# Kernel tuning notes

Measured on AMD Instinct MI355X. Metric: run time of the kernel, lower is better.

The kernel has to match this reference:

```python
import jax, jax.numpy as jnp
import numpy as np

T, B, DG, DH, S = 48, 96, 192, 384, 3
LAM, ETA = 0.9, 0.5
LN_EPS = 1e-5

def layernorm(x, g, b):
    m = jnp.mean(x, axis=-1, keepdims=True)
    v = jnp.var(x, axis=-1, keepdims=True)
    return (x - m) * jax.lax.rsqrt(v + LN_EPS) * g + b

def setup_inputs() -> dict:
    key = jax.random.key(0)
    k0, k1, k2, k3 = jax.random.split(key, 4)
    z_seq = jax.random.normal(k0, (T, B, DG), jnp.float32)
    # kaiming-uniform-ish / xavier-ish scaling for realism
    W_h = jax.random.normal(k1, (DH, DH), jnp.float32) * (2.0 / DH) ** 0.5
    W_g = jax.random.normal(k2, (DH, DG), jnp.float32) * (1.0 / DG) ** 0.5
    b_h = jnp.zeros((DH,), jnp.float32)
    ln_g = jnp.ones((DH,), jnp.float32)
    ln_b = jnp.zeros((DH,), jnp.float32)
    alpha_fw = jax.random.uniform(k3, (1,), jnp.float32)  # cfg.alpha_fw (learned scalar)
    return dict(z_seq=z_seq, W_h=W_h, W_g=W_g, b_h=b_h, ln_g=ln_g, ln_b=ln_b, alpha_fw=alpha_fw)

def reference(z_seq, W_h, W_g, b_h, ln_g, ln_b, alpha_fw):
    # compute_k(): curvature of cosine gate
    k = jnp.where(alpha_fw >= 0,
                  1.0 + jax.nn.softplus(alpha_fw),
                  1.0 / (1.0 + jax.nn.softplus(-alpha_fw)))  # shape (1,)

    def step(carry, z_t):
        h, A = carry                                   # h: [B,DH], A: [B,DH,DH]
        h_base = h @ W_h.T + z_t @ W_g.T + b_h          # [B,DH]
        h_s = jax.nn.relu(layernorm(h_base, ln_g, ln_b))
        # inner fast-weight settling loop with cosine-similarity gate
        for _ in range(S):
            Ah = jnp.einsum('bij,bj->bi', A, h_s)       # bmm(A, h)
            dot = jnp.sum(h_s * Ah, axis=-1, keepdims=True)
            n1 = jnp.maximum(jnp.linalg.norm(h_s, axis=-1, keepdims=True), 1e-6)
            n2 = jnp.maximum(jnp.linalg.norm(Ah, axis=-1, keepdims=True), 1e-6)
            R = jnp.clip(dot / (n1 * n2), 0.0, 1.0)
            a = 1.0 - (1.0 - R) ** k                    # alpha_dyn, [B,1]
            h_s = jax.nn.relu(layernorm((1.0 - a * a) * h_base + a * Ah, ln_g, ln_b))
        h = h_s
        # Hebbian fast-weight update: A <- lambda*A + eta * h h^T
        A = LAM * A + ETA * jnp.einsum('bi,bj->bij', h, h)
        return (h, A), None

    Bn, Dh = z_seq.shape[1], W_h.shape[0]
    h0 = jnp.zeros((Bn, Dh), z_seq.dtype)
    A0 = jnp.zeros((Bn, Dh, Dh), z_seq.dtype)
    (h, A), _ = jax.lax.scan(step, (h0, A0), z_seq[:-1])

    # final (query) step: no gating, no A update, h_s = relu(LN(h_base + A h_s))
    z_t = z_seq[-1]
    h_base = h @ W_h.T + z_t @ W_g.T + b_h
    h = jax.nn.relu(layernorm(h_base, ln_g, ln_b))
    for _ in range(S):
        Ah = jnp.einsum('bij,bj->bi', A, h)
        h = jax.nn.relu(layernorm(h_base + Ah, ln_g, ln_b))
    return h
```

## Files before the change

kernel.cpp:

```cpp
#include <hip/hip_runtime.h>
#include <math.h>

#define TT    48
#define BB    96
#define DG    192
#define DH    384
#define NSTEP 47
#define SETI  3
#define NT    768
#define NWAVE 12
#define NOW   6
#define NG    48

typedef unsigned short ushort_t;
typedef float f32x2 __attribute__((ext_vector_type(2)));

template <int CTRL, int RM>
__device__ __forceinline__ float dppadd(float acc, float x) {
  int t = __builtin_amdgcn_update_dpp(0, __float_as_int(x), CTRL, RM, 0xF, false);
  return acc + __int_as_float(t);
}

__device__ __forceinline__ float row16_sum(float v) {
  v = dppadd<0x128, 0xF>(v, v);
  v = dppadd<0x124, 0xF>(v, v);
  v = dppadd<0x122, 0xF>(v, v);
  v = dppadd<0x121, 0xF>(v, v);
  return v;
}

__device__ __forceinline__ float wave_sum63(float v) {
  v = row16_sum(v);
  v = dppadd<0x142, 0xA>(v, v);
  v = dppadd<0x143, 0xC>(v, v);
  return v;
}

__device__ __forceinline__ float blo(unsigned u) {
  return __uint_as_float(u << 16);
}
__device__ __forceinline__ float bhi(unsigned u) {
  return __uint_as_float(u & 0xFFFF0000u);
}
__device__ __forceinline__ f32x2 pkfma(f32x2 a, f32x2 b, f32x2 c) {
  return __builtin_elementwise_fma(a, b, c);
}

template <bool FULL>
__device__ __forceinline__ void matvec(
    const float* __restrict__ Wh_f, const float* __restrict__ Wg_f,
    const ushort_t* __restrict__ Wh_b,
    const float* __restrict__ hprev, const float* __restrict__ zsh,
    const float* __restrict__ gzrow,
    const float (&bias)[8], float* __restrict__ hbs,
    float& s1, float& s2, int g, int lane16, bool with_h)
{
  f32x2 h2[12];
  if (with_h) {
    const float4* h4 = (const float4*)hprev;
#pragma unroll
    for (int c = 0; c < 6; ++c) {
      float4 hh = h4[lane16 + 16 * c];
      h2[2 * c]     = f32x2{hh.x, hh.y};
      h2[2 * c + 1] = f32x2{hh.z, hh.w};
    }
  }
  float4 zz[3];
  if (!FULL) {
    const float4* z4 = (const float4*)zsh;
#pragma unroll
    for (int c = 0; c < 3; ++c) zz[c] = z4[lane16 + 16 * c];
  }
#pragma unroll 2
  for (int p = 0; p < 8; ++p) {
    const int r = p * NG + g;
    f32x2 acc0 = {0.f, 0.f}, acc1 = {0.f, 0.f};
    float gzv = 0.f;
    if (FULL) {
      if (lane16 == 0) gzv = gzrow[r];
    } else {
      const float4* wg = (const float4*)Wg_f + (size_t)r * (DG / 4);
#pragma unroll
      for (int c = 0; c < 3; ++c) {
        float4 w = wg[lane16 + 16 * c];
        acc0 = pkfma(f32x2{w.x, w.y}, f32x2{zz[c].x, zz[c].y}, acc0);
        acc1 = pkfma(f32x2{w.z, w.w}, f32x2{zz[c].z, zz[c].w}, acc1);
      }
    }
    if (with_h) {
      if (FULL) {
        const uint2* wh = (const uint2*)Wh_b + (size_t)r * (DH / 4);
#pragma unroll
        for (int c = 0; c < 6; ++c) {
          uint2 u = wh[lane16 + 16 * c];
          acc0 = pkfma(f32x2{blo(u.x), bhi(u.x)}, h2[2 * c], acc0);
          acc1 = pkfma(f32x2{blo(u.y), bhi(u.y)}, h2[2 * c + 1], acc1);
        }
      } else {
        const float4* wh = (const float4*)Wh_f + (size_t)r * (DH / 4);
#pragma unroll
        for (int c = 0; c < 6; ++c) {
          float4 w = wh[lane16 + 16 * c];
          acc0 = pkfma(f32x2{w.x, w.y}, h2[2 * c], acc0);
          acc1 = pkfma(f32x2{w.z, w.w}, h2[2 * c + 1], acc1);
        }
      }
    }
    float accs = row16_sum((acc0.x + acc1.x) + (acc0.y + acc1.y));
    if (lane16 == 0) {
      float vv = accs + (FULL ? gzv : bias[p]);
      hbs[r] = vv;
      s1 += vv;
      s2 += vv * vv;
    }
  }
}

template <bool FULL>
__global__ __launch_bounds__(NT) void fw_rnn_kernel(
    const float* __restrict__ z_seq,
    const float* __restrict__ Wh_f,
    const float* __restrict__ Wg_f,
    const ushort_t* __restrict__ Wh_b,
    const float* __restrict__ gz,
    const float* __restrict__ b_h,
    const float* __restrict__ ln_g,
    const float* __restrict__ ln_b,
    const float* __restrict__ alpha_fw,
    float* __restrict__ out)
{
  __shared__ __align__(16) float hs[DH];
  __shared__ __align__(16) float hbs[DH];
  __shared__ __align__(16) float zsh[DG];
  __shared__ float wlam[NSTEP];
  __shared__ __align__(16) float carr[NG];
  __shared__ __align__(16) float redA[NWAVE * 2];
  __shared__ __align__(16) float redB[2][32];

  const int tid    = threadIdx.x;
  const int b      = blockIdx.x;
  const int lane   = tid & 63, wv = tid >> 6;
  const int g      = tid >> 4, lane16 = tid & 15;
  const bool owner = (tid < DH);
  const bool zst   = (!FULL) && (tid >= DH) && (tid < DH + DG / 4);

  float bias[8];
#pragma unroll
  for (int p = 0; p < 8; ++p) bias[p] = 0.f;
  if (!FULL && lane16 == 0) {
#pragma unroll
    for (int p = 0; p < 8; ++p) bias[p] = b_h[p * NG + g];
  }
  float g_i = 0.f, be_i = 0.f;
  if (owner) { g_i = ln_g[tid]; be_i = ln_b[tid]; }

  const float af   = alpha_fw[0];
  const float kcur = (af >= 0.f) ? (1.f + log1pf(expf(af)))
                                 : (1.f / (1.f + log1pf(expf(-af))));
  const float invD = 1.0f / (float)DH;

  float hcol[48];
#pragma unroll
  for (int q = 0; q < 48; ++q) hcol[q] = 0.f;
  float4 hreg[6];
#pragma unroll
  for (int c = 0; c < 6; ++c) hreg[c] = float4{0.f, 0.f, 0.f, 0.f};

  if (!FULL && tid < DG / 4)
    ((float4*)zsh)[tid] = ((const float4*)(z_seq + (size_t)b * DG))[tid];
  if (tid < NG) carr[tid] = 0.f;
  if (tid < 2) { redB[tid][30] = 0.f; redB[tid][31] = 0.f; }
  __syncthreads();

  float Shb = 0.f, Shb2 = 0.f;

  for (int t = 0; t < NSTEP; ++t) {
    if (t > 0 && g == t - 1) {
#pragma unroll
      for (int c = 0; c < 6; ++c) hreg[c] = ((const float4*)hs)[lane16 + 16 * c];
    }
    float s1 = 0.f, s2 = 0.f;
    matvec<FULL>(Wh_f, Wg_f, Wh_b, hs, zsh,
                 FULL ? gz + ((size_t)t * BB + b) * DH : nullptr,
                 bias, hbs, s1, s2, g, lane16, t > 0);
    {
      float v0 = wave_sum63(s1);
      float v1 = wave_sum63(s2);
      if (lane == 63) { redA[wv * 2] = v0; redA[wv * 2 + 1] = v1; }
    }
    __syncthreads();

    float hb = 0.f, hsv = 0.f;
    if (owner) {
      float S1 = 0.f, S2 = 0.f;
      const float4* ra4 = (const float4*)redA;
#pragma unroll
      for (int q = 0; q < 6; ++q) {
        float4 ch = ra4[q];
        S1 += ch.x + ch.z;
        S2 += ch.y + ch.w;
      }
      Shb = S1; Shb2 = S2;
      hb = hbs[tid];
      float m   = S1 * invD;
      float var = S2 * invD - m * m;
      hsv = fmaxf((hb - m) * rsqrtf(var + 1e-5f) * g_i + be_i, 0.f);
      hs[tid] = hsv;
    }
    if (t == 0) {
      if (owner) hcol[0] = hsv;
      if (tid == 0) wlam[0] = 0.5f;
      if (zst)
        ((float4*)zsh)[tid - DH] =
            ((const float4*)(z_seq + ((size_t)1 * BB + b) * DG))[tid - DH];
      __syncthreads();
      continue;
    }
    __syncthreads();

    float4 znext;
    if (zst)
      znext = ((const float4*)(z_seq + ((size_t)(t + 1) * BB + b) * DG))[tid - DH];

    for (int s = 0; s < SETI; ++s) {
      if (g < t) {
        const float4* s4 = (const float4*)hs;
        f32x2 p0 = {0.f, 0.f}, p1 = {0.f, 0.f};
#pragma unroll
        for (int c = 0; c < 6; ++c) {
          float4 ss = s4[lane16 + 16 * c];
          p0 = pkfma(f32x2{hreg[c].x, hreg[c].y}, f32x2{ss.x, ss.y}, p0);
          p1 = pkfma(f32x2{hreg[c].z, hreg[c].w}, f32x2{ss.z, ss.w}, p1);
        }
        float p = row16_sum((p0.x + p1.x) + (p0.y + p1.y));
        if (lane16 == 0) carr[g] = p * wlam[g];
      }
      __syncthreads();

      float ah = 0.f;
      if (owner) {
        const float4* c4 = (const float4*)carr;
        float ah0 = 0.f, ah1 = 0.f, ah2 = 0.f, ah3 = 0.f;
#pragma unroll
        for (int q = 0; q < 12; ++q) {
          float4 c = c4[q];
          ah0 = fmaf(c.x, hcol[4 * q + 0], ah0);
          ah1 = fmaf(c.y, hcol[4 * q + 1], ah1);
          ah2 = fmaf(c.z, hcol[4 * q + 2], ah2);
          ah3 = fmaf(c.w, hcol[4 * q + 3], ah3);
        }
        ah = (ah0 + ah2) + (ah1 + ah3);
        float v0 = wave_sum63(hsv * ah);
        float v1 = wave_sum63(hsv * hsv);
        float v2 = wave_sum63(ah * ah);
        float v3 = wave_sum63(hb * ah);
        float v4 = wave_sum63(ah);
        if (lane == 63) {
          float* rb = redB[s & 1];
          rb[wv * 5 + 0] = v0; rb[wv * 5 + 1] = v1; rb[wv * 5 + 2] = v2;
          rb[wv * 5 + 3] = v3; rb[wv * 5 + 4] = v4;
        }
      }
      __syncthreads();

      if (owner) {
        const float4* rb4 = (const float4*)redB[s & 1];
        float S[5] = {0.f, 0.f, 0.f, 0.f, 0.f};
#pragma unroll
        for (int q = 0; q < 8; ++q) {
          float4 ch = rb4[q];
          S[(4 * q + 0) % 5] += ch.x;
          S[(4 * q + 1) % 5] += ch.y;
          S[(4 * q + 2) % 5] += ch.z;
          S[(4 * q + 3) % 5] += ch.w;
        }
        float n1 = fmaxf(sqrtf(S[1]), 1e-6f);
        float n2 = fmaxf(sqrtf(S[2]), 1e-6f);
        float R  = fminf(fmaxf(__fdividef(S[0], n1 * n2), 0.f), 1.f);
        float a  = 1.f - __expf(kcur * __logf(1.f - R));
        float beta = 1.f - a * a;
        float mu  = (beta * Shb + a * S[4]) * invD;
        float Exx = (beta * beta * Shb2 + 2.f * beta * a * S[3] + a * a * S[2]) * invD;
        float var = Exx - mu * mu;
        float xv  = beta * hb + a * ah;
        hsv = fmaxf((xv - mu) * rsqrtf(var + 1e-5f) * g_i + be_i, 0.f);
        hs[tid] = hsv;
        if (s == SETI - 1) {
#pragma unroll
          for (int q = 0; q < 48; ++q)
            if (q == t) hcol[q] = hsv;
        }
      }
      if (s == SETI - 1) {
        if (tid < t) wlam[tid] *= 0.9f;
        else if (tid == t) wlam[tid] = 0.5f;
        if (zst) ((float4*)zsh)[tid - DH] = znext;
      }
      __syncthreads();
    }
  }

  {
    if (g == NSTEP - 1) {
#pragma unroll
      for (int c = 0; c < 6; ++c) hreg[c] = ((const float4*)hs)[lane16 + 16 * c];
    }
    float s1 = 0.f, s2 = 0.f;
    matvec<FULL>(Wh_f, Wg_f, Wh_b, hs, zsh,
                 FULL ? gz + ((size_t)NSTEP * BB + b) * DH : nullptr,
                 bias, hbs, s1, s2, g, lane16, true);
    {
      float v0 = wave_sum63(s1);
      float v1 = wave_sum63(s2);
      if (lane == 63) { redA[wv * 2] = v0; redA[wv * 2 + 1] = v1; }
    }
    __syncthreads();

    float hb = 0.f, hv = 0.f;
    if (owner) {
      float S1 = 0.f, S2 = 0.f;
      const float4* ra4 = (const float4*)redA;
#pragma unroll
      for (int q = 0; q < 6; ++q) {
        float4 ch = ra4[q];
        S1 += ch.x + ch.z;
        S2 += ch.y + ch.w;
      }
      Shb = S1; Shb2 = S2;
      hb = hbs[tid];
      float m   = S1 * invD;
      float var = S2 * invD - m * m;
      hv = fmaxf((hb - m) * rsqrtf(var + 1e-5f) * g_i + be_i, 0.f);
      hs[tid] = hv;
    }
    __syncthreads();

    for (int s = 0; s < SETI; ++s) {
      if (g < NSTEP) {
        const float4* s4 = (const float4*)hs;
        f32x2 p0 = {0.f, 0.f}, p1 = {0.f, 0.f};
#pragma unroll
        for (int c = 0; c < 6; ++c) {
          float4 ss = s4[lane16 + 16 * c];
          p0 = pkfma(f32x2{hreg[c].x, hreg[c].y}, f32x2{ss.x, ss.y}, p0);
          p1 = pkfma(f32x2{hreg[c].z, hreg[c].w}, f32x2{ss.z, ss.w}, p1);
        }
        float p = row16_sum((p0.x + p1.x) + (p0.y + p1.y));
        if (lane16 == 0) carr[g] = p * wlam[g];
      }
      __syncthreads();

      float ah = 0.f;
      if (owner) {
        const float4* c4 = (const float4*)carr;
        float ah0 = 0.f, ah1 = 0.f, ah2 = 0.f, ah3 = 0.f;
#pragma unroll
        for (int q = 0; q < 12; ++q) {
          float4 c = c4[q];
          ah0 = fmaf(c.x, hcol[4 * q + 0], ah0);
          ah1 = fmaf(c.y, hcol[4 * q + 1], ah1);
          ah2 = fmaf(c.z, hcol[4 * q + 2], ah2);
          ah3 = fmaf(c.w, hcol[4 * q + 3], ah3);
        }
        ah = (ah0 + ah2) + (ah1 + ah3);
        float v0 = wave_sum63(ah);
        float v1 = wave_sum63(ah * ah);
        float v2 = wave_sum63(hb * ah);
        if (lane == 63) {
          float* rb = redB[s & 1];
          rb[wv * 5 + 0] = v0; rb[wv * 5 + 1] = v1; rb[wv * 5 + 2] = v2;
        }
      }
      __syncthreads();

      if (owner) {
        const float4* rb4 = (const float4*)redB[s & 1];
        float S[5] = {0.f, 0.f, 0.f, 0.f, 0.f};
#pragma unroll
        for (int q = 0; q < 8; ++q) {
          float4 ch = rb4[q];
          S[(4 * q + 0) % 5] += ch.x;
          S[(4 * q + 1) % 5] += ch.y;
          S[(4 * q + 2) % 5] += ch.z;
          S[(4 * q + 3) % 5] += ch.w;
        }
        float Sx  = Shb + S[0];
        float Sxx = Shb2 + 2.f * S[2] + S[1];
        float mu  = Sx * invD;
        float var = Sxx * invD - mu * mu;
        float xv  = hb + ah;
        hv = fmaxf((xv - mu) * rsqrtf(var + 1e-5f) * g_i + be_i, 0.f);
        if (s < SETI - 1) hs[tid] = hv;
      }
      if (s < SETI - 1) __syncthreads();
    }

    if (owner) out[(size_t)b * DH + tid] = hv;
  }
}

__global__ __launch_bounds__(NT) void gz_kernel(
    const float* __restrict__ z_seq, const ushort_t* __restrict__ Wg_b,
    const float* __restrict__ b_h, float* __restrict__ gz)
{
  __shared__ __align__(16) float zsh[DG];
  const int tid = threadIdx.x, b = blockIdx.x, t = blockIdx.y;
  const int g = tid >> 4, lane16 = tid & 15;
  if (tid < DG / 4)
    ((float4*)zsh)[tid] = ((const float4*)(z_seq + ((size_t)t * BB + b) * DG))[tid];
  __syncthreads();
  float4 zz[3];
  const float4* z4 = (const float4*)zsh;
#pragma unroll
  for (int c = 0; c < 3; ++c) zz[c] = z4[lane16 + 16 * c];
  float* grow = gz + ((size_t)t * BB + b) * DH;
#pragma unroll
  for (int p = 0; p < 8; ++p) {
    const int r = p * NG + g;
    const uint2* wg = (const uint2*)Wg_b + (size_t)r * (DG / 4);
    f32x2 acc0 = {0.f, 0.f}, acc1 = {0.f, 0.f};
#pragma unroll
    for (int c = 0; c < 3; ++c) {
      uint2 u = wg[lane16 + 16 * c];
      acc0 = pkfma(f32x2{blo(u.x), bhi(u.x)}, f32x2{zz[c].x, zz[c].y}, acc0);
      acc1 = pkfma(f32x2{blo(u.y), bhi(u.y)}, f32x2{zz[c].z, zz[c].w}, acc1);
    }
    float a = row16_sum((acc0.x + acc1.x) + (acc0.y + acc1.y));
    if (lane16 == 0) grow[r] = a + b_h[r];
  }
}

__global__ void cvt_kernel(const float* __restrict__ src,
                           ushort_t* __restrict__ dst, int n) {
  int i = blockIdx.x * blockDim.x + threadIdx.x;
  if (i < n) {
    unsigned u = __float_as_uint(src[i]);
    unsigned r = (u + 0x7FFFu + ((u >> 16) & 1u)) >> 16;
    dst[i] = (ushort_t)r;
  }
}

extern "C" void kernel_launch(void* const* d_in, const int* in_sizes, int n_in,
                              void* d_out, int out_size, void* d_ws, size_t ws_size,
                              hipStream_t stream) {
  const float* z_seq    = (const float*)d_in[0];
  const float* W_h      = (const float*)d_in[1];
  const float* W_g      = (const float*)d_in[2];
  const float* b_h      = (const float*)d_in[3];
  const float* ln_g     = (const float*)d_in[4];
  const float* ln_b     = (const float*)d_in[5];
  const float* alpha_fw = (const float*)d_in[6];
  float* out = (float*)d_out;

  const size_t nWh = (size_t)DH * DH;
  const size_t nWg = (size_t)DH * DG;
  const size_t bf16Bytes = (nWh + nWg) * sizeof(ushort_t);
  const size_t gzBytes   = (size_t)TT * BB * DH * sizeof(float);

  if (ws_size >= bf16Bytes + gzBytes) {
    ushort_t* Whb = (ushort_t*)d_ws;
    ushort_t* Wgb = Whb + nWh;
    float* gz = (float*)((char*)d_ws + bf16Bytes);
    cvt_kernel<<<dim3((int)((nWh + 255) / 256)), dim3(256), 0, stream>>>(
        W_h, Whb, (int)nWh);
    cvt_kernel<<<dim3((int)((nWg + 255) / 256)), dim3(256), 0, stream>>>(
        W_g, Wgb, (int)nWg);
    gz_kernel<<<dim3(BB, TT), dim3(NT), 0, stream>>>(z_seq, Wgb, b_h, gz);
    fw_rnn_kernel<true><<<dim3(BB), dim3(NT), 0, stream>>>(
        z_seq, W_h, W_g, Whb, gz, b_h, ln_g, ln_b, alpha_fw, out);
  } else {
    fw_rnn_kernel<false><<<dim3(BB), dim3(NT), 0, stream>>>(
        z_seq, W_h, W_g, nullptr, nullptr, b_h, ln_g, ln_b, alpha_fw, out);
  }
}
```

Before: 573.8 us.

## Keep half of W_h in registers, move hidden history to LDS, batch gz kernel

The recurrent kernel now loads half of each thread's bf16 W_h rows into registers once and reloads only the other half each step. Rows are remapped so each group owns 8 contiguous rows, which allows vectorized hbs and gz accesses, and next-step gz values are prefetched. The per-thread 48-entry hidden-history register array is replaced by a padded transposed LDS buffer, which removes the dynamic-index select loop. The gz kernel now keeps fp32 W_g in registers across 6 timesteps per block, so the W_g bf16 conversion launch is dropped. The trade-off is higher register pressure in the main kernel and a large LDS allocation (about 80 KB).

```diff
diff --git a/kernel.cpp b/kernel.cpp
--- a/kernel.cpp
+++ b/kernel.cpp
@@ -5,6 +5,7 @@
 #define BB    96
 #define DG    192
 #define DH    384
+#define HSTR  52
 #define NSTEP 47
 #define SETI  3
 #define NT    768
@@ -46,18 +47,61 @@
   return __builtin_elementwise_fma(a, b, c);
 }
 
-template <bool FULL>
-__device__ __forceinline__ void matvec(
+__device__ __forceinline__ void matvec_full(
+    const uint2 (&wreg)[24], const ushort_t* __restrict__ Wh_b,
+    const float* __restrict__ hs, const float (&gzv)[8],
+    float* __restrict__ hbs, float& s1, float& s2,
+    int g, int lane16, bool with_h)
+{
+  float rs[8];
+  if (with_h) {
+    uint2 uw[24];
+#pragma unroll
+    for (int p = 0; p < 4; ++p)
+#pragma unroll
+      for (int c = 0; c < 6; ++c)
+        uw[p * 6 + c] =
+            ((const uint2*)Wh_b)[(size_t)(8 * g + 4 + p) * (DH / 4) + lane16 + 16 * c];
+    f32x2 h2[12];
+    const float4* h4 = (const float4*)hs;
+#pragma unroll
+    for (int c = 0; c < 6; ++c) {
+      float4 hh = h4[lane16 + 16 * c];
+      h2[2 * c]     = f32x2{hh.x, hh.y};
+      h2[2 * c + 1] = f32x2{hh.z, hh.w};
+    }
+#pragma unroll
+    for (int p = 0; p < 8; ++p) {
+      f32x2 a0 = {0.f, 0.f}, a1 = {0.f, 0.f};
+#pragma unroll
+      for (int c = 0; c < 6; ++c) {
+        uint2 u = (p < 4) ? wreg[p * 6 + c] : uw[(p - 4) * 6 + c];
+        a0 = pkfma(f32x2{blo(u.x), bhi(u.x)}, h2[2 * c], a0);
+        a1 = pkfma(f32x2{blo(u.y), bhi(u.y)}, h2[2 * c + 1], a1);
+      }
+      rs[p] = row16_sum((a0.x + a1.x) + (a0.y + a1.y)) + gzv[p];
+    }
+  } else {
+#pragma unroll
+    for (int p = 0; p < 8; ++p) rs[p] = gzv[p];
+  }
+  if (lane16 == 0) {
+#pragma unroll
+    for (int p = 0; p < 8; ++p) { s1 += rs[p]; s2 += rs[p] * rs[p]; }
+    ((float4*)(hbs + 8 * g))[0] = float4{rs[0], rs[1], rs[2], rs[3]};
+    ((float4*)(hbs + 8 * g))[1] = float4{rs[4], rs[5], rs[6], rs[7]};
+  }
+}
+
+__device__ __forceinline__ void matvec_ref(
     const float* __restrict__ Wh_f, const float* __restrict__ Wg_f,
-    const ushort_t* __restrict__ Wh_b,
-    const float* __restrict__ hprev, const float* __restrict__ zsh,
-    const float* __restrict__ gzrow,
+    const float* __restrict__ hs, const float* __restrict__ zsh,
     const float (&bias)[8], float* __restrict__ hbs,
     float& s1, float& s2, int g, int lane16, bool with_h)
 {
   f32x2 h2[12];
   if (with_h) {
-    const float4* h4 = (const float4*)hprev;
+    const float4* h4 = (const float4*)hs;
 #pragma unroll
     for (int c = 0; c < 6; ++c) {
       float4 hh = h4[lane16 + 16 * c];
@@ -66,53 +110,37 @@
     }
   }
   float4 zz[3];
-  if (!FULL) {
-    const float4* z4 = (const float4*)zsh;
-#pragma unroll
-    for (int c = 0; c < 3; ++c) zz[c] = z4[lane16 + 16 * c];
-  }
-#pragma unroll 2
+  const float4* z4 = (const float4*)zsh;
+#pragma unroll
+  for (int c = 0; c < 3; ++c) zz[c] = z4[lane16 + 16 * c];
+  float rs[8];
+#pragma unroll
   for (int p = 0; p < 8; ++p) {
-    const int r = p * NG + g;
-    f32x2 acc0 = {0.f, 0.f}, acc1 = {0.f, 0.f};
-    float gzv = 0.f;
-    if (FULL) {
-      if (lane16 == 0) gzv = gzrow[r];
-    } else {
-      const float4* wg = (const float4*)Wg_f + (size_t)r * (DG / 4);
-#pragma unroll
-      for (int c = 0; c < 3; ++c) {
-        float4 w = wg[lane16 + 16 * c];
-        acc0 = pkfma(f32x2{w.x, w.y}, f32x2{zz[c].x, zz[c].y}, acc0);
-        acc1 = pkfma(f32x2{w.z, w.w}, f32x2{zz[c].z, zz[c].w}, acc1);
-      }
+    const int r = 8 * g + p;
+    f32x2 a0 = {0.f, 0.f}, a1 = {0.f, 0.f};
+    const float4* wg = (const float4*)Wg_f + (size_t)r * (DG / 4);
+#pragma unroll
+    for (int c = 0; c < 3; ++c) {
+      float4 w = wg[lane16 + 16 * c];
+      a0 = pkfma(f32x2{w.x, w.y}, f32x2{zz[c].x, zz[c].y}, a0);
+      a1 = pkfma(f32x2{w.z, w.w}, f32x2{zz[c].z, zz[c].w}, a1);
     }
     if (with_h) {
-      if (FULL) {
-        const uint2* wh = (const uint2*)Wh_b + (size_t)r * (DH / 4);
-#pragma unroll
-        for (int c = 0; c < 6; ++c) {
-          uint2 u = wh[lane16 + 16 * c];
-          acc0 = pkfma(f32x2{blo(u.x), bhi(u.x)}, h2[2 * c], acc0);
-          acc1 = pkfma(f32x2{blo(u.y), bhi(u.y)}, h2[2 * c + 1], acc1);
-        }
-      } else {
-        const float4* wh = (const float4*)Wh_f + (size_t)r * (DH / 4);
-#pragma unroll
-        for (int c = 0; c < 6; ++c) {
-          float4 w = wh[lane16 + 16 * c];
-          acc0 = pkfma(f32x2{w.x, w.y}, h2[2 * c], acc0);
-          acc1 = pkfma(f32x2{w.z, w.w}, h2[2 * c + 1], acc1);
-        }
-      }
-    }
-    float accs = row16_sum((acc0.x + acc1.x) + (acc0.y + acc1.y));
-    if (lane16 == 0) {
-      float vv = accs + (FULL ? gzv : bias[p]);
-      hbs[r] = vv;
-      s1 += vv;
-      s2 += vv * vv;
-    }
+      const float4* wh = (const float4*)Wh_f + (size_t)r * (DH / 4);
+#pragma unroll
+      for (int c = 0; c < 6; ++c) {
+        float4 w = wh[lane16 + 16 * c];
+        a0 = pkfma(f32x2{w.x, w.y}, h2[2 * c], a0);
+        a1 = pkfma(f32x2{w.z, w.w}, h2[2 * c + 1], a1);
+      }
+    }
+    rs[p] = row16_sum((a0.x + a1.x) + (a0.y + a1.y)) + bias[p];
+  }
+  if (lane16 == 0) {
+#pragma unroll
+    for (int p = 0; p < 8; ++p) { s1 += rs[p]; s2 += rs[p] * rs[p]; }
+    ((float4*)(hbs + 8 * g))[0] = float4{rs[0], rs[1], rs[2], rs[3]};
+    ((float4*)(hbs + 8 * g))[1] = float4{rs[4], rs[5], rs[6], rs[7]};
   }
 }
 
@@ -129,6 +157,7 @@
     const float* __restrict__ alpha_fw,
     float* __restrict__ out)
 {
+  __shared__ __align__(16) float histT[DH * HSTR];
   __shared__ __align__(16) float hs[DH];
   __shared__ __align__(16) float hbs[DH];
   __shared__ __align__(16) float zsh[DG];
@@ -144,12 +173,22 @@
   const bool owner = (tid < DH);
   const bool zst   = (!FULL) && (tid >= DH) && (tid < DH + DG / 4);
 
+  uint2 wreg[24];
+  if (FULL) {
+#pragma unroll
+    for (int p = 0; p < 4; ++p)
+#pragma unroll
+      for (int c = 0; c < 6; ++c)
+        wreg[p * 6 + c] =
+            ((const uint2*)Wh_b)[(size_t)(8 * g + p) * (DH / 4) + lane16 + 16 * c];
+  }
+
   float bias[8];
 #pragma unroll
   for (int p = 0; p < 8; ++p) bias[p] = 0.f;
   if (!FULL && lane16 == 0) {
 #pragma unroll
-    for (int p = 0; p < 8; ++p) bias[p] = b_h[p * NG + g];
+    for (int p = 0; p < 8; ++p) bias[p] = b_h[8 * g + p];
   }
   float g_i = 0.f, be_i = 0.f;
   if (owner) { g_i = ln_g[tid]; be_i = ln_b[tid]; }
@@ -159,30 +198,44 @@
                                  : (1.f / (1.f + log1pf(expf(-af))));
   const float invD = 1.0f / (float)DH;
 
-  float hcol[48];
-#pragma unroll
-  for (int q = 0; q < 48; ++q) hcol[q] = 0.f;
-  float4 hreg[6];
-#pragma unroll
-  for (int c = 0; c < 6; ++c) hreg[c] = float4{0.f, 0.f, 0.f, 0.f};
-
+  float4 gzc0 = {0.f, 0.f, 0.f, 0.f}, gzc1 = {0.f, 0.f, 0.f, 0.f};
+  if (FULL && lane16 == 0) {
+    const float4* gp = (const float4*)(gz + (size_t)b * DH + 8 * g);
+    gzc0 = gp[0]; gzc1 = gp[1];
+  }
+
+  for (int i = tid; i < DH * HSTR / 4; i += NT)
+    ((float4*)histT)[i] = float4{0.f, 0.f, 0.f, 0.f};
   if (!FULL && tid < DG / 4)
     ((float4*)zsh)[tid] = ((const float4*)(z_seq + (size_t)b * DG))[tid];
   if (tid < NG) carr[tid] = 0.f;
   if (tid < 2) { redB[tid][30] = 0.f; redB[tid][31] = 0.f; }
   __syncthreads();
 
+  float4 hreg[6];
+#pragma unroll
+  for (int c = 0; c < 6; ++c) hreg[c] = float4{0.f, 0.f, 0.f, 0.f};
+
   float Shb = 0.f, Shb2 = 0.f;
 
   for (int t = 0; t < NSTEP; ++t) {
+    float4 gzn0 = {0.f, 0.f, 0.f, 0.f}, gzn1 = {0.f, 0.f, 0.f, 0.f};
+    if (FULL && lane16 == 0) {
+      const float4* gp = (const float4*)(gz + ((size_t)(t + 1) * BB + b) * DH + 8 * g);
+      gzn0 = gp[0]; gzn1 = gp[1];
+    }
+    float gzv[8] = {gzc0.x, gzc0.y, gzc0.z, gzc0.w, gzc1.x, gzc1.y, gzc1.z, gzc1.w};
+
+    float s1 = 0.f, s2 = 0.f;
+    if (FULL)
+      matvec_full(wreg, Wh_b, hs, gzv, hbs, s1, s2, g, lane16, t > 0);
+    else
+      matvec_ref(Wh_f, Wg_f, hs, zsh, bias, hbs, s1, s2, g, lane16, t > 0);
+
     if (t > 0 && g == t - 1) {
 #pragma unroll
       for (int c = 0; c < 6; ++c) hreg[c] = ((const float4*)hs)[lane16 + 16 * c];
     }
-    float s1 = 0.f, s2 = 0.f;
-    matvec<FULL>(Wh_f, Wg_f, Wh_b, hs, zsh,
-                 FULL ? gz + ((size_t)t * BB + b) * DH : nullptr,
-                 bias, hbs, s1, s2, g, lane16, t > 0);
     {
       float v0 = wave_sum63(s1);
       float v1 = wave_sum63(s2);
@@ -208,11 +261,12 @@
       hs[tid] = hsv;
     }
     if (t == 0) {
-      if (owner) hcol[0] = hsv;
+      if (owner) histT[tid * HSTR] = hsv;
       if (tid == 0) wlam[0] = 0.5f;
       if (zst)
         ((float4*)zsh)[tid - DH] =
             ((const float4*)(z_seq + ((size_t)1 * BB + b) * DG))[tid - DH];
+      gzc0 = gzn0; gzc1 = gzn1;
       __syncthreads();
       continue;
     }
@@ -239,17 +293,19 @@
 
       float ah = 0.f;
       if (owner) {
+        const float4* hT = (const float4*)(histT + tid * HSTR);
         const float4* c4 = (const float4*)carr;
-        float ah0 = 0.f, ah1 = 0.f, ah2 = 0.f, ah3 = 0.f;
+        float a0 = 0.f, a1 = 0.f, a2 = 0.f, a3 = 0.f;
 #pragma unroll
         for (int q = 0; q < 12; ++q) {
-          float4 c = c4[q];
-          ah0 = fmaf(c.x, hcol[4 * q + 0], ah0);
-          ah1 = fmaf(c.y, hcol[4 * q + 1], ah1);
-          ah2 = fmaf(c.z, hcol[4 * q + 2], ah2);
-          ah3 = fmaf(c.w, hcol[4 * q + 3], ah3);
-        }
-        ah = (ah0 + ah2) + (ah1 + ah3);
+          float4 hv4 = hT[q];
+          float4 cc  = c4[q];
+          a0 = fmaf(cc.x, hv4.x, a0);
+          a1 = fmaf(cc.y, hv4.y, a1);
+          a2 = fmaf(cc.z, hv4.z, a2);
+          a3 = fmaf(cc.w, hv4.w, a3);
+        }
+        ah = (a0 + a2) + (a1 + a3);
         float v0 = wave_sum63(hsv * ah);
         float v1 = wave_sum63(hsv * hsv);
         float v2 = wave_sum63(ah * ah);
@@ -285,11 +341,7 @@
         float xv  = beta * hb + a * ah;
         hsv = fmaxf((xv - mu) * rsqrtf(var + 1e-5f) * g_i + be_i, 0.f);
         hs[tid] = hsv;
-        if (s == SETI - 1) {
-#pragma unroll
-          for (int q = 0; q < 48; ++q)
-            if (q == t) hcol[q] = hsv;
-        }
+        if (s == SETI - 1) histT[tid * HSTR + t] = hsv;
       }
       if (s == SETI - 1) {
         if (tid < t) wlam[tid] *= 0.9f;
@@ -298,17 +350,20 @@
       }
       __syncthreads();
     }
+    gzc0 = gzn0; gzc1 = gzn1;
   }
 
   {
+    float gzv[8] = {gzc0.x, gzc0.y, gzc0.z, gzc0.w, gzc1.x, gzc1.y, gzc1.z, gzc1.w};
+    float s1 = 0.f, s2 = 0.f;
+    if (FULL)
+      matvec_full(wreg, Wh_b, hs, gzv, hbs, s1, s2, g, lane16, true);
+    else
+      matvec_ref(Wh_f, Wg_f, hs, zsh, bias, hbs, s1, s2, g, lane16, true);
     if (g == NSTEP - 1) {
 #pragma unroll
       for (int c = 0; c < 6; ++c) hreg[c] = ((const float4*)hs)[lane16 + 16 * c];
     }
-    float s1 = 0.f, s2 = 0.f;
-    matvec<FULL>(Wh_f, Wg_f, Wh_b, hs, zsh,
-                 FULL ? gz + ((size_t)NSTEP * BB + b) * DH : nullptr,
-                 bias, hbs, s1, s2, g, lane16, true);
     {
       float v0 = wave_sum63(s1);
       float v1 = wave_sum63(s2);
@@ -352,17 +407,19 @@
 
       float ah = 0.f;
       if (owner) {
+        const float4* hT = (const float4*)(histT + tid * HSTR);
         const float4* c4 = (const float4*)carr;
-        float ah0 = 0.f, ah1 = 0.f, ah2 = 0.f, ah3 = 0.f;
+        float a0 = 0.f, a1 = 0.f, a2 = 0.f, a3 = 0.f;
 #pragma unroll
         for (int q = 0; q < 12; ++q) {
-          float4 c = c4[q];
-          ah0 = fmaf(c.x, hcol[4 * q + 0], ah0);
-          ah1 = fmaf(c.y, hcol[4 * q + 1], ah1);
-          ah2 = fmaf(c.z, hcol[4 * q + 2], ah2);
-          ah3 = fmaf(c.w, hcol[4 * q + 3], ah3);
-        }
-        ah = (ah0 + ah2) + (ah1 + ah3);
+          float4 hv4 = hT[q];
+          float4 cc  = c4[q];
+          a0 = fmaf(cc.x, hv4.x, a0);
+          a1 = fmaf(cc.y, hv4.y, a1);
+          a2 = fmaf(cc.z, hv4.z, a2);
+          a3 = fmaf(cc.w, hv4.w, a3);
+        }
+        ah = (a0 + a2) + (a1 + a3);
         float v0 = wave_sum63(ah);
         float v1 = wave_sum63(ah * ah);
         float v2 = wave_sum63(hb * ah);
@@ -400,33 +457,48 @@
 }
 
 __global__ __launch_bounds__(NT) void gz_kernel(
-    const float* __restrict__ z_seq, const ushort_t* __restrict__ Wg_b,
+    const float* __restrict__ z_seq, const float* __restrict__ Wg,
     const float* __restrict__ b_h, float* __restrict__ gz)
 {
   __shared__ __align__(16) float zsh[DG];
-  const int tid = threadIdx.x, b = blockIdx.x, t = blockIdx.y;
+  const int tid = threadIdx.x, b = blockIdx.x;
   const int g = tid >> 4, lane16 = tid & 15;
-  if (tid < DG / 4)
-    ((float4*)zsh)[tid] = ((const float4*)(z_seq + ((size_t)t * BB + b) * DG))[tid];
-  __syncthreads();
-  float4 zz[3];
-  const float4* z4 = (const float4*)zsh;
-#pragma unroll
-  for (int c = 0; c < 3; ++c) zz[c] = z4[lane16 + 16 * c];
-  float* grow = gz + ((size_t)t * BB + b) * DH;
-#pragma unroll
-  for (int p = 0; p < 8; ++p) {
-    const int r = p * NG + g;
-    const uint2* wg = (const uint2*)Wg_b + (size_t)r * (DG / 4);
-    f32x2 acc0 = {0.f, 0.f}, acc1 = {0.f, 0.f};
-#pragma unroll
-    for (int c = 0; c < 3; ++c) {
-      uint2 u = wg[lane16 + 16 * c];
-      acc0 = pkfma(f32x2{blo(u.x), bhi(u.x)}, f32x2{zz[c].x, zz[c].y}, acc0);
-      acc1 = pkfma(f32x2{blo(u.y), bhi(u.y)}, f32x2{zz[c].z, zz[c].w}, acc1);
-    }
-    float a = row16_sum((acc0.x + acc1.x) + (acc0.y + acc1.y));
-    if (lane16 == 0) grow[r] = a + b_h[r];
+  float4 w[24];
+#pragma unroll
+  for (int p = 0; p < 8; ++p)
+#pragma unroll
+    for (int c = 0; c < 3; ++c)
+      w[p * 3 + c] = ((const float4*)Wg)[(size_t)(8 * g + p) * (DG / 4) + lane16 + 16 * c];
+  float4 bs0 = {0.f, 0.f, 0.f, 0.f}, bs1 = {0.f, 0.f, 0.f, 0.f};
+  if (lane16 == 0) {
+    bs0 = ((const float4*)b_h)[2 * g];
+    bs1 = ((const float4*)b_h)[2 * g + 1];
+  }
+  for (int tt = 0; tt < 6; ++tt) {
+    const int t = blockIdx.y * 6 + tt;
+    __syncthreads();
+    if (tid < DG / 4)
+      ((float4*)zsh)[tid] = ((const float4*)(z_seq + ((size_t)t * BB + b) * DG))[tid];
+    __syncthreads();
+    float4 zz[3];
+#pragma unroll
+    for (int c = 0; c < 3; ++c) zz[c] = ((const float4*)zsh)[lane16 + 16 * c];
+    float rs[8];
+#pragma unroll
+    for (int p = 0; p < 8; ++p) {
+      f32x2 a0 = {0.f, 0.f}, a1 = {0.f, 0.f};
+#pragma unroll
+      for (int c = 0; c < 3; ++c) {
+        a0 = pkfma(f32x2{w[p * 3 + c].x, w[p * 3 + c].y}, f32x2{zz[c].x, zz[c].y}, a0);
+        a1 = pkfma(f32x2{w[p * 3 + c].z, w[p * 3 + c].w}, f32x2{zz[c].z, zz[c].w}, a1);
+      }
+      rs[p] = row16_sum((a0.x + a1.x) + (a0.y + a1.y));
+    }
+    if (lane16 == 0) {
+      float* grow = gz + ((size_t)t * BB + b) * DH + 8 * g;
+      ((float4*)grow)[0] = float4{rs[0] + bs0.x, rs[1] + bs0.y, rs[2] + bs0.z, rs[3] + bs0.w};
+      ((float4*)grow)[1] = float4{rs[4] + bs1.x, rs[5] + bs1.y, rs[6] + bs1.z, rs[7] + bs1.w};
+    }
   }
 }
 
@@ -453,19 +525,15 @@
   float* out = (float*)d_out;
 
   const size_t nWh = (size_t)DH * DH;
-  const size_t nWg = (size_t)DH * DG;
-  const size_t bf16Bytes = (nWh + nWg) * sizeof(ushort_t);
+  const size_t bf16Bytes = nWh * sizeof(ushort_t);
   const size_t gzBytes   = (size_t)TT * BB * DH * sizeof(float);
 
   if (ws_size >= bf16Bytes + gzBytes) {
     ushort_t* Whb = (ushort_t*)d_ws;
-    ushort_t* Wgb = Whb + nWh;
     float* gz = (float*)((char*)d_ws + bf16Bytes);
     cvt_kernel<<<dim3((int)((nWh + 255) / 256)), dim3(256), 0, stream>>>(
         W_h, Whb, (int)nWh);
-    cvt_kernel<<<dim3((int)((nWg + 255) / 256)), dim3(256), 0, stream>>>(
-        W_g, Wgb, (int)nWg);
-    gz_kernel<<<dim3(BB, TT), dim3(NT), 0, stream>>>(z_seq, Wgb, b_h, gz);
+    gz_kernel<<<dim3(BB, 8), dim3(NT), 0, stream>>>(z_seq, W_g, b_h, gz);
     fw_rnn_kernel<true><<<dim3(BB), dim3(NT), 0, stream>>>(
         z_seq, W_h, W_g, Whb, gz, b_h, ln_g, ln_b, alpha_fw, out);
   } else {
```

After: 762.3 us. +32.8%, slower.
